# Kernel tuning notes

Hardware: AMD Instinct MI355X
Metric: run time of the kernel (lower is better)

## Reference

```python
import jax, jax.numpy as jnp
import numpy as np
from jax import lax

DIM = 512
HEADS = 8
HID = 128           # FRN hidden_dim
DIM_CONV = DIM // 4 # 128, partial-conv channels
EPS = 1e-5


def layernorm(x, g, b):
    mu = jnp.mean(x, axis=-1, keepdims=True)
    var = jnp.mean((x - mu) ** 2, axis=-1, keepdims=True)
    return (x - mu) * lax.rsqrt(var + EPS) * g + b


def conv2d(x, w, groups=1):
    # x: (N,C,H,W), w: (O, C/groups, kh, kw), stride 1, SAME padding
    return lax.conv_general_dilated(x, w, (1, 1), 'SAME',
                                    dimension_numbers=('NCHW', 'OIHW', 'NCHW'),
                                    feature_group_count=groups)


def setup_inputs() -> dict:
    key = jax.random.key(0)
    ks = jax.random.split(key, 12)
    s = 0.02
    inp = {
        'x': jax.random.normal(ks[0], (196, 256, DIM), dtype=jnp.float32),
        'ln1_g': jnp.ones((DIM,), jnp.float32),
        'ln1_b': jnp.zeros((DIM,), jnp.float32),
        'qkv_w': jax.random.normal(ks[1], (DIM, 3 * DIM), jnp.float32) * s,
        'proj_w': jax.random.normal(ks[2], (DIM, DIM), jnp.float32) * s,
        'proj_b': jnp.zeros((DIM,), jnp.float32),
        'ln2_g': jnp.ones((DIM,), jnp.float32),
        'ln2_b': jnp.zeros((DIM,), jnp.float32),
        'pconv_w': jax.random.normal(ks[3], (DIM_CONV, DIM_CONV, 3, 3), jnp.float32) * s,
        'lin1_w': jax.random.normal(ks[4], (DIM, 2 * HID), jnp.float32) * s,
        'lin1_b': jnp.zeros((2 * HID,), jnp.float32),
        'dw_w': jax.random.normal(ks[5], (HID, 1, 3, 3), jnp.float32) * s,
        'dw_b': jnp.zeros((HID,), jnp.float32),
        'lin2_w': jax.random.normal(ks[6], (HID, DIM), jnp.float32) * s,
        'lin2_b': jnp.zeros((DIM,), jnp.float32),
    }
    return inp


def reference(x, ln1_g, ln1_b, qkv_w, proj_w, proj_b, ln2_g, ln2_b,
              pconv_w, lin1_w, lin1_b, dw_w, dw_b, lin2_w, lin2_b):
    B, N, C = x.shape
    hd = C // HEADS
    scale = hd ** -0.5

    # ---- SQAttention on norm1(x) ----
    h = layernorm(x, ln1_g, ln1_b)
    qkv = (h @ qkv_w).reshape(B, N, 3, HEADS, hd)
    q, k, v = qkv[:, :, 0], qkv[:, :, 1], qkv[:, :, 2]  # (B,N,H,hd)
    attn = jnp.einsum('bnhd,bmhd->bhnm', q, k) * scale   # (B,H,N,N)
    # sigmoid mask from the LAST query row, averaged over heads
    mask = jax.nn.sigmoid(jnp.mean(attn[:, :, -1, :], axis=1))[:, None, None, :]  # (B,1,1,N)
    attn = jax.nn.softmax(attn, axis=-1) * mask
    o = jnp.einsum('bhnm,bmhd->bnhd', attn, v).reshape(B, N, C)
    x = x + (o @ proj_w + proj_b)

    # ---- FRN on norm2(x): treats axis0 as (h w)=hw, axis1 as batch ----
    y = layernorm(x, ln2_g, ln2_b)
    hw, bs, c = y.shape
    hh = int(np.sqrt(hw))
    yi = y.reshape(hh, hh, bs, c).transpose(2, 3, 0, 1)  # (bs,c,hh,hh)
    y1 = conv2d(yi[:, :DIM_CONV], pconv_w)               # partial conv, no bias
    yi = jnp.concatenate([y1, yi[:, DIM_CONV:]], axis=1)
    y = yi.transpose(2, 3, 0, 1).reshape(hw, bs, c)      # (hw,bs,c)
    y = jax.nn.gelu(y @ lin1_w + lin1_b, approximate=False)
    y_1, y_2 = y[..., :HID], y[..., HID:]
    y1i = y_1.reshape(hh, hh, bs, HID).transpose(2, 3, 0, 1)
    y1i = jax.nn.gelu(conv2d(y1i, dw_w, groups=HID) + dw_b[None, :, None, None],
                      approximate=False)
    y_1 = y1i.transpose(2, 3, 0, 1).reshape(hw, bs, HID)
    y = (y_1 * y_2) @ lin2_w + lin2_b
    return x + y
```

## Files before the change

### kernel.cpp

```cpp
#include <hip/hip_runtime.h>
#include <hip/hip_bf16.h>

#define NB   196
#define NT   256
#define CDIM 512
#define NH   8
#define MROWS 50176
#define HB   98
#define MH   (HB*NT)

typedef __attribute__((ext_vector_type(8))) short short8;
typedef __attribute__((ext_vector_type(4))) float f32x4;
typedef __attribute__((ext_vector_type(4))) unsigned uint32x4;

__device__ __forceinline__ float gelu_f(float x) {
    return 0.5f * x * (1.0f + erff(x * 0.70710678118654752440f));
}
__device__ __forceinline__ float b2f(unsigned u) { return __uint_as_float(u << 16); }
__device__ __forceinline__ unsigned f2b(float f) {
    __hip_bfloat16 h = __float2bfloat16(f);
    return (unsigned)__builtin_bit_cast(unsigned short, h);
}
__device__ __forceinline__ unsigned pk2(float a, float b) { return f2b(a) | (f2b(b) << 16); }
__device__ __forceinline__ void u4_to_f8(uint4 v, float* f) {
    f[0] = b2f(v.x & 0xffffu); f[1] = b2f(v.x >> 16);
    f[2] = b2f(v.y & 0xffffu); f[3] = b2f(v.y >> 16);
    f[4] = b2f(v.z & 0xffffu); f[5] = b2f(v.z >> 16);
    f[6] = b2f(v.w & 0xffffu); f[7] = b2f(v.w >> 16);
}
__device__ __forceinline__ void gload_lds16(const void* g, void* l) {
    __builtin_amdgcn_global_load_lds(
        (const __attribute__((address_space(1))) void*)g,
        (__attribute__((address_space(3))) void*)l, 16, 0, 0);
}
static inline int xcd_grid(int NBM, int NBN) { return 8 * ((NBM + 7) / 8) * NBN; }

__global__ __launch_bounds__(256) void convert_wT_kernel(
    const float* __restrict__ w, unsigned short* __restrict__ wT, int K, int N)
{
    int o = blockIdx.x * 256 + threadIdx.x;
    if (o >= K * N) return;
    int k = o / N, n = o - k * N;
    wT[(size_t)n * K + k] = (unsigned short)f2b(w[o]);
}
__global__ __launch_bounds__(256) void convert_kernel(
    const float* __restrict__ w, unsigned short* __restrict__ wT, int n)
{
    int o = blockIdx.x * 256 + threadIdx.x;
    if (o < n) wT[o] = (unsigned short)f2b(w[o]);
}

template<int INBF>
__global__ __launch_bounds__(64) void ln_kernel(
    const void* __restrict__ inp, const float* __restrict__ g,
    const float* __restrict__ b, unsigned short* __restrict__ out)
{
    int row = blockIdx.x;
    int lane = threadIdx.x;
    float f[8];
    if constexpr (INBF) {
        const unsigned short* p = (const unsigned short*)inp + (size_t)row * CDIM + lane * 8;
        uint4 v = *(const uint4*)p;
        u4_to_f8(v, f);
    } else {
        const float* p = (const float*)inp + (size_t)row * CDIM + lane * 8;
        float4 a = *(const float4*)p;
        float4 c = *(const float4*)(p + 4);
        f[0]=a.x; f[1]=a.y; f[2]=a.z; f[3]=a.w; f[4]=c.x; f[5]=c.y; f[6]=c.z; f[7]=c.w;
    }
    float s = 0;
#pragma unroll
    for (int i = 0; i < 8; ++i) s += f[i];
#pragma unroll
    for (int off = 1; off < 64; off <<= 1) s += __shfl_xor(s, off);
    float mu = s * (1.0f / 512.0f);
    float sq = 0;
#pragma unroll
    for (int i = 0; i < 8; ++i) { f[i] -= mu; sq += f[i] * f[i]; }
#pragma unroll
    for (int off = 1; off < 64; off <<= 1) sq += __shfl_xor(sq, off);
    float inv = rsqrtf(sq * (1.0f / 512.0f) + 1e-5f);
    float4 g0 = *(const float4*)(g + lane * 8);
    float4 g1 = *(const float4*)(g + lane * 8 + 4);
    float4 b0 = *(const float4*)(b + lane * 8);
    float4 b1 = *(const float4*)(b + lane * 8 + 4);
    float r0 = f[0]*inv*g0.x + b0.x, r1 = f[1]*inv*g0.y + b0.y;
    float r2 = f[2]*inv*g0.z + b0.z, r3 = f[3]*inv*g0.w + b0.w;
    float r4 = f[4]*inv*g1.x + b1.x, r5 = f[5]*inv*g1.y + b1.y;
    float r6 = f[6]*inv*g1.z + b1.z, r7 = f[7]*inv*g1.w + b1.w;
    uint4 ov = { pk2(r0, r1), pk2(r2, r3), pk2(r4, r5), pk2(r6, r7) };
    *(uint4*)(out + (size_t)row * CDIM + lane * 8) = ov;
}

#define QUAD16(MH, NH) \
    __builtin_amdgcn_s_setprio(1); \
    _Pragma("unroll") \
    for (int mi2 = 0; mi2 < 4; ++mi2) \
        _Pragma("unroll") \
        for (int nj2 = 0; nj2 < 2; ++nj2) \
            _Pragma("unroll") \
            for (int kk = 0; kk < 2; ++kk) \
                acc[(MH)*4 + mi2][(NH)*2 + nj2] = __builtin_amdgcn_mfma_f32_16x16x32_bf16( \
                    afr[mi2][kk], bfr[nj2][kk], acc[(MH)*4 + mi2][(NH)*2 + nj2], 0, 0, 0); \
    __builtin_amdgcn_s_setprio(0);

template<typename TC, int RES>
__global__ __launch_bounds__(512, 2) void gemm_mfma256(
    const unsigned short* __restrict__ A,
    const unsigned short* __restrict__ BT,
    const float* __restrict__ bias,
    const void* __restrict__ resid,
    TC* __restrict__ C,
    int K, int lda, int ldc, int act, int NBM, int NBN)
{
    __shared__ __align__(16) unsigned short As[2][256][64];
    __shared__ __align__(16) unsigned short Bs[2][256][64];
    int lin = blockIdx.x;
    int xcd = lin & 7;
    int rr = lin >> 3;
    int nb = rr % NBN;
    int pb = rr / NBN;
    int mb = (pb << 3) + xcd;
    if (mb >= NBM) return;
    int m0 = mb << 8;
    int n0 = nb << 8;

    int tid = threadIdx.x;
    int lane = tid & 63;
    int wave = tid >> 6;
    int wr = wave >> 2;
    int wc = wave & 3;
    int fr = lane & 15;
    int fg = lane >> 4;

    int rsub8 = lane >> 3;
    int cch = lane & 7;

    auto stage = [&](int p, int k0) {
#pragma unroll
        for (int tI = 0; tI < 4; ++tI) {
            int seg = (wave << 2) + tI;
            int row = (seg << 3) + rsub8;
            int csrc = (cch ^ (row & 7)) << 3;
            gload_lds16(A + (size_t)(m0 + row) * lda + k0 + csrc,
                        (char*)&As[p][0][0] + (seg << 10));
        }
#pragma unroll
        for (int tI = 0; tI < 4; ++tI) {
            int seg = (wave << 2) + tI;
            int row = (seg << 3) + rsub8;
            int csrc = (cch ^ (row & 7)) << 3;
            gload_lds16(BT + (size_t)(n0 + row) * K + k0 + csrc,
                        (char*)&Bs[p][0][0] + (seg << 10));
        }
    };

    f32x4 acc[8][4];
#pragma unroll
    for (int i = 0; i < 8; ++i)
#pragma unroll
        for (int j = 0; j < 4; ++j) acc[i][j] = (f32x4){0.f, 0.f, 0.f, 0.f};

    short8 afr[4][2];
    short8 bfr[2][2];

    auto loadA = [&](int p, int mh) {
#pragma unroll
        for (int mi2 = 0; mi2 < 4; ++mi2)
#pragma unroll
            for (int kk = 0; kk < 2; ++kk) {
                int row = (wr << 7) + (mh << 6) + (mi2 << 4) + fr;
                int ch = ((kk << 2) + fg) ^ (row & 7);
                afr[mi2][kk] = *(const short8*)&As[p][row][ch << 3];
            }
    };
    auto loadB = [&](int p, int nh) {
#pragma unroll
        for (int nj2 = 0; nj2 < 2; ++nj2)
#pragma unroll
            for (int kk = 0; kk < 2; ++kk) {
                int row = (wc << 6) + (nh << 5) + (nj2 << 4) + fr;
                int ch = ((kk << 2) + fg) ^ (row & 7);
                bfr[nj2][kk] = *(const short8*)&Bs[p][row][ch << 3];
            }
    };

    int NKT = K >> 6;
    stage(0, 0);
    asm volatile("s_waitcnt vmcnt(0)" ::: "memory");
    __builtin_amdgcn_s_barrier();

    for (int t = 0; t < NKT; ++t) {
        int p = t & 1;
        if (t + 1 < NKT) stage(p ^ 1, (t + 1) << 6);
        loadA(p, 0); loadB(p, 0);
        QUAD16(0, 0)
        __builtin_amdgcn_s_barrier();
        loadB(p, 1);
        QUAD16(0, 1)
        __builtin_amdgcn_s_barrier();
        loadA(p, 1);
        QUAD16(1, 1)
        __builtin_amdgcn_s_barrier();
        loadB(p, 0);
        QUAD16(1, 0)
        if (t + 1 < NKT) asm volatile("s_waitcnt vmcnt(0)" ::: "memory");
        __builtin_amdgcn_s_barrier();
    }

#pragma unroll
    for (int mi = 0; mi < 8; ++mi) {
        int rowb = m0 + (wr << 7) + (mi << 4) + (fg << 2);
#pragma unroll
        for (int nj = 0; nj < 4; ++nj) {
            int col = n0 + (wc << 6) + (nj << 4) + fr;
            float bj = bias ? bias[col] : 0.0f;
#pragma unroll
            for (int r = 0; r < 4; ++r) {
                int row = rowb + r;
                float v = acc[mi][nj][r] + bj;
                if constexpr (RES == 1)
                    v += ((const float*)resid)[(size_t)row * ldc + col];
                else if constexpr (RES == 2)
                    v += b2f(((const unsigned short*)resid)[(size_t)row * ldc + col]);
                if (act) v = gelu_f(v);
                if constexpr (sizeof(TC) == 4)
                    ((float*)C)[(size_t)row * ldc + col] = v;
                else
                    ((unsigned short*)C)[(size_t)row * ldc + col] = (unsigned short)f2b(v);
            }
        }
    }
}

template<typename TC, int RES, int CONV>
__global__ __launch_bounds__(256) void gemm_mfma(
    const unsigned short* __restrict__ A,
    const unsigned short* __restrict__ BT,
    const float* __restrict__ bias,
    const void* __restrict__ resid,
    TC* __restrict__ C,
    int K, int lda, int ldc, int act, int NBM, int NBN)
{
    __shared__ __align__(16) unsigned short As[3][128][32];
    __shared__ __align__(16) unsigned short Bs[3][128][32];
    int lin = blockIdx.x;
    int xcd = lin & 7;
    int rr = lin >> 3;
    int nb = rr % NBN;
    int pb = rr / NBN;
    int mb = (pb << 3) + xcd;
    if (mb >= NBM) return;
    int m0 = mb << 7;
    int n0 = nb << 7;

    int tid = threadIdx.x;
    int lane = tid & 63;
    int wave = tid >> 6;
    int wr = wave >> 1, wc = wave & 1;
    int fr = lane & 15;
    int fg = lane >> 4;

    int rsub = lane >> 2;
    int cch = lane & 3;
    int csrc = (cch ^ (rsub & 3)) << 3;

    int i0 = 0, j0 = 0, bs0 = 0;
    if constexpr (CONV) {
        int hw = m0 >> 8;
        i0 = hw / 14; j0 = hw - i0 * 14;
        bs0 = m0 & 255;
    }

    auto stage = [&](int bf, int k0) {
        if constexpr (CONV) {
            int kl = tid & 31;
            int mq = (tid >> 5) << 4;
            int k = k0 + kl;
            int ci = k / 9; int r9 = k - ci * 9;
            int di = r9 / 3; int dj = r9 - di * 3;
            int ii = i0 + di - 1, jj = j0 + dj - 1;
            uint4 v0 = {0,0,0,0}, v1 = {0,0,0,0};
            if ((unsigned)ii < 14u && (unsigned)jj < 14u) {
                const unsigned short* src = A + (size_t)ci * MROWS + (size_t)(ii * 14 + jj) * 256 + bs0 + mq;
                v0 = *(const uint4*)src;
                v1 = *(const uint4*)(src + 8);
            }
            unsigned short e[16];
            *(uint4*)&e[0] = v0; *(uint4*)&e[8] = v1;
            int ch = kl >> 3, wi = kl & 7;
#pragma unroll
            for (int e2 = 0; e2 < 16; ++e2)
                As[bf][mq + e2][((ch ^ (e2 & 3)) << 3) + wi] = e[e2];
        } else {
#pragma unroll
            for (int t = 0; t < 2; ++t) {
                int seg = (wave << 1) + t;
                int row = (seg << 4) + rsub;
                gload_lds16(A + (size_t)(m0 + row) * lda + k0 + csrc,
                            (char*)&As[bf][0][0] + (seg << 10));
            }
        }
#pragma unroll
        for (int t = 0; t < 2; ++t) {
            int seg = (wave << 1) + t;
            int row = (seg << 4) + rsub;
            gload_lds16(BT + (size_t)(n0 + row) * K + k0 + csrc,
                        (char*)&Bs[bf][0][0] + (seg << 10));
        }
    };

    f32x4 acc[4][4];
#pragma unroll
    for (int i = 0; i < 4; ++i)
#pragma unroll
        for (int j = 0; j < 4; ++j) acc[i][j] = (f32x4){0.f, 0.f, 0.f, 0.f};

    int nsteps = K >> 5;
    stage(0, 0);
    if (nsteps > 1) {
        stage(1, 32);
        asm volatile("s_waitcnt vmcnt(4)" ::: "memory");
    } else {
        asm volatile("s_waitcnt vmcnt(0)" ::: "memory");
    }
    __builtin_amdgcn_s_barrier();

    for (int s = 0; s < nsteps; ++s) {
        int bcur = s % 3;
        if (s + 2 < nsteps) stage((s + 2) % 3, (s + 2) << 5);
        int chl = (fg ^ (fr & 3)) << 3;
        short8 af[4], bfr[4];
#pragma unroll
        for (int i = 0; i < 4; ++i)
            af[i] = *(const short8*)&As[bcur][(wr << 6) + (i << 4) + fr][chl];
#pragma unroll
        for (int j = 0; j < 4; ++j)
            bfr[j] = *(const short8*)&Bs[bcur][(wc << 6) + (j << 4) + fr][chl];
#pragma unroll
        for (int i = 0; i < 4; ++i)
#pragma unroll
            for (int j = 0; j < 4; ++j)
                acc[i][j] = __builtin_amdgcn_mfma_f32_16x16x32_bf16(af[i], bfr[j], acc[i][j], 0, 0, 0);
        if (s + 1 < nsteps) {
            if (s + 2 < nsteps) asm volatile("s_waitcnt vmcnt(4) lgkmcnt(0)" ::: "memory");
            else                asm volatile("s_waitcnt vmcnt(0) lgkmcnt(0)" ::: "memory");
            __builtin_amdgcn_s_barrier();
        }
    }

#pragma unroll
    for (int i = 0; i < 4; ++i) {
        int rowb = m0 + (wr << 6) + (i << 4) + ((lane >> 4) << 2);
#pragma unroll
        for (int j = 0; j < 4; ++j) {
            int col = n0 + (wc << 6) + (j << 4) + fr;
            float bj = bias ? bias[col] : 0.0f;
#pragma unroll
            for (int r = 0; r < 4; ++r) {
                int row = rowb + r;
                float v = acc[i][j][r] + bj;
                if constexpr (RES == 1)
                    v += ((const float*)resid)[(size_t)row * ldc + col];
                else if constexpr (RES == 2)
                    v += b2f(((const unsigned short*)resid)[(size_t)row * ldc + col]);
                if (act) v = gelu_f(v);
                if constexpr (sizeof(TC) == 4)
                    ((float*)C)[(size_t)row * ldc + col] = v;
                else
                    ((unsigned short*)C)[(size_t)row * ldc + col] = (unsigned short)f2b(v);
            }
        }
    }
}

__global__ __launch_bounds__(256) void mask_kernel(
    const unsigned short* __restrict__ qkv, float* __restrict__ mk)
{
    __shared__ float ql[512];
    int b = blockIdx.x, tid = threadIdx.x;
    const unsigned short* qlast = qkv + ((size_t)(b * NT + 255) * 3) * CDIM;
    ql[tid] = b2f(qlast[tid]);
    ql[tid + 256] = b2f(qlast[tid + 256]);
    __syncthreads();
    const unsigned short* kp = qkv + ((size_t)(b * NT + tid) * 3 + 1) * CDIM;
    float s = 0;
    for (int cq = 0; cq < 512; cq += 8) {
        uint4 kv = *(const uint4*)(kp + cq);
        float f[8];
        u4_to_f8(kv, f);
#pragma unroll
        for (int q = 0; q < 8; ++q) s += ql[cq + q] * f[q];
    }
    s *= 0.015625f;
    mk[b * NT + tid] = 1.0f / (1.0f + __expf(-s));
}

__global__ __launch_bounds__(512) void attn_mfma(
    const unsigned short* __restrict__ qkv, const float* __restrict__ mask,
    unsigned short* __restrict__ o)
{
    __shared__ __align__(16) unsigned short smem[128][64];
    int h = blockIdx.x, b = blockIdx.y;
    int tid = threadIdx.x;
    int lane = tid & 63;
    int wid = tid >> 6;
    int fr = lane & 15;
    int fg = lane >> 4;
    const unsigned short* base = qkv + (size_t)b * NT * 3 * CDIM + h * 64;

    short8 qf[2][2];
#pragma unroll
    for (int t = 0; t < 2; ++t)
#pragma unroll
        for (int kc = 0; kc < 2; ++kc)
            qf[t][kc] = *(const short8*)(base +
                (size_t)((wid << 5) + (t << 4) + fr) * 3 * CDIM + (kc << 5) + (fg << 3));

    f32x4 oacc[2][4];
#pragma unroll
    for (int t = 0; t < 2; ++t)
#pragma unroll
        for (int n = 0; n < 4; ++n) oacc[t][n] = (f32x4){0.f, 0.f, 0.f, 0.f};
    float l[2] = {0.f, 0.f};

    int srcA = ((fg & 1) << 5) + fr;

    for (int c = 0; c < 4; ++c) {
        __syncthreads();
        {
            int kr = tid >> 3, ch = tid & 7;
            int gm = (c << 6) + kr;
            uint4 kv = *(const uint4*)(base + (size_t)(gm * 3 + 1) * CDIM + (ch << 3));
            *(uint4*)&smem[kr][(ch ^ (kr & 7)) << 3] = kv;
            float mv = mask[b * NT + gm];
            uint4 vv = *(const uint4*)(base + (size_t)(gm * 3 + 2) * CDIM + (ch << 3));
            float f[8];
            u4_to_f8(vv, f);
#pragma unroll
            for (int e = 0; e < 8; ++e) {
                int d = (ch << 3) + e;
                smem[64 + d][(((kr >> 3) ^ (d & 7)) << 3) + (kr & 7)] = (unsigned short)f2b(f[e] * mv);
            }
        }
        __syncthreads();
        short8 kf[4][2];
#pragma unroll
        for (int j = 0; j < 4; ++j)
#pragma unroll
            for (int kc = 0; kc < 2; ++kc)
                kf[j][kc] = *(const short8*)&smem[(j << 4) + fr][((((kc << 2) + fg) ^ (fr & 7)) << 3)];
        short8 vf[4][2];
#pragma unroll
        for (int n = 0; n < 4; ++n)
#pragma unroll
            for (int kc2 = 0; kc2 < 2; ++kc2)
                vf[n][kc2] = *(const short8*)&smem[64 + (n << 4) + fr][((((kc2 << 2) + fg) ^ (fr & 7)) << 3)];
#pragma unroll
        for (int t = 0; t < 2; ++t) {
            f32x4 sa[4];
#pragma unroll
            for (int j = 0; j < 4; ++j) sa[j] = (f32x4){0.f, 0.f, 0.f, 0.f};
#pragma unroll
            for (int kc = 0; kc < 2; ++kc)
#pragma unroll
                for (int j = 0; j < 4; ++j)
                    sa[j] = __builtin_amdgcn_mfma_f32_16x16x32_bf16(kf[j][kc], qf[t][kc], sa[j], 0, 0, 0);
            float p[4][4];
            float ls = 0.f;
#pragma unroll
            for (int j = 0; j < 4; ++j)
#pragma unroll
                for (int r = 0; r < 4; ++r) {
                    p[j][r] = __expf(sa[j][r] * 0.125f);
                    ls += p[j][r];
                }
            ls += __shfl_xor(ls, 16);
            ls += __shfl_xor(ls, 32);
            l[t] += ls;
            unsigned pkv[4][2];
#pragma unroll
            for (int j = 0; j < 4; ++j) {
                pkv[j][0] = pk2(p[j][0], p[j][1]);
                pkv[j][1] = pk2(p[j][2], p[j][3]);
            }
#pragma unroll
            for (int kc2 = 0; kc2 < 2; ++kc2) {
                unsigned w0[4], w1[4];
                w0[0] = __shfl(pkv[(kc2 << 1) + 0][0], srcA);
                w0[1] = __shfl(pkv[(kc2 << 1) + 0][1], srcA);
                w0[2] = __shfl(pkv[(kc2 << 1) + 0][0], srcA + 16);
                w0[3] = __shfl(pkv[(kc2 << 1) + 0][1], srcA + 16);
                w1[0] = __shfl(pkv[(kc2 << 1) + 1][0], srcA);
                w1[1] = __shfl(pkv[(kc2 << 1) + 1][1], srcA);
                w1[2] = __shfl(pkv[(kc2 << 1) + 1][0], srcA + 16);
                w1[3] = __shfl(pkv[(kc2 << 1) + 1][1], srcA + 16);
                bool hi = fg >= 2;
                uint32x4 pw = { hi ? w1[0] : w0[0], hi ? w1[1] : w0[1],
                                hi ? w1[2] : w0[2], hi ? w1[3] : w0[3] };
                short8 pf = __builtin_bit_cast(short8, pw);
#pragma unroll
                for (int n = 0; n < 4; ++n)
                    oacc[t][n] = __builtin_amdgcn_mfma_f32_16x16x32_bf16(pf, vf[n][kc2], oacc[t][n], 0, 0, 0);
            }
        }
    }

#pragma unroll
    for (int half = 0; half < 2; ++half) {
        __syncthreads();
        if ((wid >> 2) == half) {
            int qr = (wid & 3) << 5;
#pragma unroll
            for (int t = 0; t < 2; ++t) {
                float invl = 1.0f / l[t];
                float rl[4];
#pragma unroll
                for (int r = 0; r < 4; ++r)
                    rl[r] = __shfl(invl, (fg << 2) + r);
#pragma unroll
                for (int n = 0; n < 4; ++n)
#pragma unroll
                    for (int r = 0; r < 4; ++r) {
                        int row = qr + (t << 4) + (fg << 2) + r;
                        int d = (n << 4) + fr;
                        smem[row][((((d >> 3) ^ (row & 7)) << 3)) | (d & 7)] =
                            (unsigned short)f2b(oacc[t][n][r] * rl[r]);
                    }
            }
        }
        __syncthreads();
#pragma unroll
        for (int p = 0; p < 2; ++p) {
            int idx = tid + (p << 9);
            int row = idx >> 3;
            int ch = idx & 7;
            uint4 ov = *(const uint4*)&smem[row][(ch ^ (row & 7)) << 3];
            *(uint4*)(o + (size_t)(b * NT + (half << 7) + row) * CDIM + h * 64 + (ch << 3)) = ov;
        }
    }
}

__global__ __launch_bounds__(256) void transpose_kernel(
    const unsigned short* __restrict__ y, unsigned short* __restrict__ yT)
{
    int g = blockIdx.x * 256 + threadIdx.x;
    int row = g >> 4;
    int cq = (g & 15) << 3;
    uint4 v = *(const uint4*)(y + (size_t)row * CDIM + cq);
    unsigned short e[8] = {
        (unsigned short)(v.x & 0xffffu), (unsigned short)(v.x >> 16),
        (unsigned short)(v.y & 0xffffu), (unsigned short)(v.y >> 16),
        (unsigned short)(v.z & 0xffffu), (unsigned short)(v.z >> 16),
        (unsigned short)(v.w & 0xffffu), (unsigned short)(v.w >> 16) };
    int hw = row >> 8, bs = row & 255;
    size_t off = (size_t)cq * MROWS + (size_t)hw * 256 + bs;
#pragma unroll
    for (int i = 0; i < 8; ++i) yT[off + (size_t)i * MROWS] = e[i];
}

__global__ __launch_bounds__(256) void dwconv_kernel(
    const unsigned short* __restrict__ u, const float* __restrict__ w,
    const float* __restrict__ wb, unsigned short* __restrict__ y1)
{
    int hw = blockIdx.x;
    int i = hw / 14;
    int j = hw - i * 14;
    int tid = threadIdx.x;
    int c = (tid & 31) << 2;
    int bs = (blockIdx.y << 3) + (tid >> 5);
    float a0 = 0, a1 = 0, a2 = 0, a3 = 0;
#pragma unroll
    for (int di = 0; di < 3; ++di) {
        int ii = i + di - 1;
        if ((unsigned)ii >= 14u) continue;
#pragma unroll
        for (int dj = 0; dj < 3; ++dj) {
            int jj = j + dj - 1;
            if ((unsigned)jj >= 14u) continue;
            int r = di * 3 + dj;
            uint2 uv = *(const uint2*)(u + ((size_t)(ii * 14 + jj) * 256 + bs) * 256 + c);
            a0 += w[(c + 0) * 9 + r] * b2f(uv.x & 0xffffu);
            a1 += w[(c + 1) * 9 + r] * b2f(uv.x >> 16);
            a2 += w[(c + 2) * 9 + r] * b2f(uv.y & 0xffffu);
            a3 += w[(c + 3) * 9 + r] * b2f(uv.y >> 16);
        }
    }
    a0 = gelu_f(a0 + wb[c]);
    a1 = gelu_f(a1 + wb[c + 1]);
    a2 = gelu_f(a2 + wb[c + 2]);
    a3 = gelu_f(a3 + wb[c + 3]);
    uint2 g2 = *(const uint2*)(u + ((size_t)hw * 256 + bs) * 256 + 128 + c);
    a0 *= b2f(g2.x & 0xffffu); a1 *= b2f(g2.x >> 16);
    a2 *= b2f(g2.y & 0xffffu); a3 *= b2f(g2.y >> 16);
    ushort4 ov = { (unsigned short)f2b(a0), (unsigned short)f2b(a1),
                   (unsigned short)f2b(a2), (unsigned short)f2b(a3) };
    *(ushort4*)(y1 + ((size_t)hw * 256 + bs) * 128 + c) = ov;
}

extern "C" void kernel_launch(void* const* d_in, const int* in_sizes, int n_in,
                              void* d_out, int out_size, void* d_ws, size_t ws_size,
                              hipStream_t stream)
{
    (void)in_sizes; (void)n_in; (void)out_size; (void)ws_size;
    const float* x      = (const float*)d_in[0];
    const float* ln1_g  = (const float*)d_in[1];
    const float* ln1_b  = (const float*)d_in[2];
    const float* qkv_w  = (const float*)d_in[3];
    const float* proj_w = (const float*)d_in[4];
    const float* proj_b = (const float*)d_in[5];
    const float* ln2_g  = (const float*)d_in[6];
    const float* ln2_b  = (const float*)d_in[7];
    const float* pconv_w= (const float*)d_in[8];
    const float* lin1_w = (const float*)d_in[9];
    const float* lin1_b = (const float*)d_in[10];
    const float* dw_w   = (const float*)d_in[11];
    const float* dw_b   = (const float*)d_in[12];
    const float* lin2_w = (const float*)d_in[13];
    const float* lin2_b = (const float*)d_in[14];
    float* out = (float*)d_out;

    unsigned short* Ob   = (unsigned short*)d_out;
    unsigned short* o_bf = Ob;
    unsigned short* h_bf = Ob + 25690112;
    float* mk            = (float*)(Ob + 25690112 + 12845056);
    unsigned short* y_bf = Ob;
    unsigned short* yT_b = Ob + 25690112;

    unsigned short* ws16   = (unsigned short*)d_ws;
    unsigned short* qkvW   = ws16;
    unsigned short* projW  = ws16 + 786432;
    unsigned short* pconvW = ws16 + 1048576;
    unsigned short* lin1W  = ws16 + 1196032;
    unsigned short* lin2W  = ws16 + 1327104;
    unsigned short* qkv_b  = ws16 + 1392640;
    unsigned short* x2_b   = ws16 + 1392640;
    unsigned short* u_b    = ws16 + 27082752;
    unsigned short* y1_b   = ws16 + 39927808;

    convert_wT_kernel<<<3072, 256, 0, stream>>>(qkv_w,  qkvW,  512, 1536);
    convert_wT_kernel<<<1024, 256, 0, stream>>>(proj_w, projW, 512, 512);
    convert_kernel  <<< 576, 256, 0, stream>>>(pconv_w, pconvW, 147456);
    convert_wT_kernel<<< 512, 256, 0, stream>>>(lin1_w, lin1W, 512, 256);
    convert_wT_kernel<<< 256, 256, 0, stream>>>(lin2_w, lin2W, 128, 512);

    for (int r = 0; r < 2; ++r) {
        const float* xr = x + (size_t)r * MH * CDIM;
        ln_kernel<0><<<MH, 64, 0, stream>>>(xr, ln1_g, ln1_b, h_bf);
        gemm_mfma256<unsigned short, 0><<<xcd_grid(98, 6), 512, 0, stream>>>(
            h_bf, qkvW, nullptr, nullptr, qkv_b, 512, 512, 1536, 0, 98, 6);
        mask_kernel<<<HB, 256, 0, stream>>>(qkv_b, mk + (size_t)r * HB * NT);
        attn_mfma<<<dim3(NH, HB), 512, 0, stream>>>(
            qkv_b, mk + (size_t)r * HB * NT, o_bf + (size_t)r * MH * CDIM);
    }
    gemm_mfma256<unsigned short, 1><<<xcd_grid(196, 2), 512, 0, stream>>>(
        o_bf, projW, proj_b, x, x2_b, 512, 512, 512, 0, 196, 2);
    ln_kernel<1><<<MROWS, 64, 0, stream>>>(x2_b, ln2_g, ln2_b, y_bf);
    transpose_kernel<<<3136, 256, 0, stream>>>(y_bf, yT_b);
    gemm_mfma<unsigned short, 0, 1><<<xcd_grid(392, 1), 256, 0, stream>>>(
        yT_b, pconvW, nullptr, nullptr, y_bf, 1152, 0, 512, 0, 392, 1);
    gemm_mfma256<unsigned short, 0><<<xcd_grid(196, 1), 512, 0, stream>>>(
        y_bf, lin1W, lin1_b, nullptr, u_b, 512, 512, 256, 1, 196, 1);
    dwconv_kernel<<<dim3(NB, 32), 256, 0, stream>>>(u_b, dw_w, dw_b, y1_b);
    gemm_mfma256<float, 2><<<xcd_grid(196, 2), 512, 0, stream>>>(
        y1_b, lin2W, lin2_b, x2_b, out, 128, 128, 512, 0, 196, 2);
}
```

Baseline: 855.1 us.

## Split next-tile global-to-LDS staging into four chunks interleaved with MFMA phases

Prefetching of the next K tile is broken into four chunks: the two A halves and the two B halves. Each chunk is issued in a different compute phase, and the phase barriers become partial `vmcnt(4)` waits, so a phase only waits for the data it actually consumes. This replaces a full `vmcnt(0)` drain at the end of every iteration, with the aim of spreading memory traffic evenly and overlapping it with MFMA work. Launch bounds also drop from 2 to 1 blocks per CU, which gives the compiler more registers; the 128 KB of LDS per block already limited occupancy to one block.

Measured after the change: 895.7 us. 1.05x slower.

```diff
diff --git a/kernel.cpp b/kernel.cpp
--- a/kernel.cpp
+++ b/kernel.cpp
@@ -104,8 +104,13 @@
                     afr[mi2][kk], bfr[nj2][kk], acc[(MH)*4 + mi2][(NH)*2 + nj2], 0, 0, 0); \
     __builtin_amdgcn_s_setprio(0);
 
+#define PHASE_WAIT() \
+    if (pre) asm volatile("s_waitcnt vmcnt(4)" ::: "memory"); \
+    else     asm volatile("s_waitcnt vmcnt(0)" ::: "memory"); \
+    __builtin_amdgcn_s_barrier();
+
 template<typename TC, int RES>
-__global__ __launch_bounds__(512, 2) void gemm_mfma256(
+__global__ __launch_bounds__(512, 1) void gemm_mfma256(
     const unsigned short* __restrict__ A,
     const unsigned short* __restrict__ BT,
     const float* __restrict__ bias,
@@ -133,25 +138,25 @@
     int fr = lane & 15;
     int fg = lane >> 4;
 
-    int rsub8 = lane >> 3;
-    int cch = lane & 7;
-
-    auto stage = [&](int p, int k0) {
-#pragma unroll
-        for (int tI = 0; tI < 4; ++tI) {
-            int seg = (wave << 2) + tI;
-            int row = (seg << 3) + rsub8;
-            int csrc = (cch ^ (row & 7)) << 3;
-            gload_lds16(A + (size_t)(m0 + row) * lda + k0 + csrc,
-                        (char*)&As[p][0][0] + (seg << 10));
-        }
-#pragma unroll
-        for (int tI = 0; tI < 4; ++tI) {
-            int seg = (wave << 2) + tI;
-            int row = (seg << 3) + rsub8;
-            int csrc = (cch ^ (row & 7)) << 3;
-            gload_lds16(BT + (size_t)(n0 + row) * K + k0 + csrc,
-                        (char*)&Bs[p][0][0] + (seg << 10));
+    auto stage_chunk = [&](int p, int k0, int type) {
+        const unsigned short* SRC;
+        char* LBASE;
+        int seg, ld, base0;
+        if (type == 0 || type == 3) {
+            SRC = A; LBASE = (char*)&As[p][0][0]; ld = lda; base0 = m0;
+            seg = (type == 0) ? ((wave < 4) ? wave : wave + 4)
+                              : ((wave < 4) ? wave + 4 : wave + 8);
+        } else {
+            SRC = BT; LBASE = (char*)&Bs[p][0][0]; ld = K; base0 = n0;
+            seg = ((wave >> 1) << 2) + (wave & 1) + ((type == 2) ? 2 : 0);
+        }
+#pragma unroll
+        for (int i = 0; i < 2; ++i) {
+            int row = (seg << 4) + (i << 3) + (lane >> 3);
+            int c = lane & 7;
+            int csrc = ((c ^ (row & 7)) << 3);
+            gload_lds16(SRC + (size_t)(base0 + row) * ld + k0 + csrc,
+                        LBASE + (seg << 11) + (i << 10));
         }
     };
 
@@ -186,26 +191,31 @@
     };
 
     int NKT = K >> 6;
-    stage(0, 0);
-    asm volatile("s_waitcnt vmcnt(0)" ::: "memory");
+    stage_chunk(0, 0, 0); stage_chunk(0, 0, 1);
+    stage_chunk(0, 0, 2); stage_chunk(0, 0, 3);
+    asm volatile("s_waitcnt vmcnt(4)" ::: "memory");
     __builtin_amdgcn_s_barrier();
 
     for (int t = 0; t < NKT; ++t) {
         int p = t & 1;
-        if (t + 1 < NKT) stage(p ^ 1, (t + 1) << 6);
+        bool pre = (t + 1 < NKT);
+        int k1 = (t + 1) << 6;
+        if (pre) stage_chunk(p ^ 1, k1, 0);
         loadA(p, 0); loadB(p, 0);
         QUAD16(0, 0)
-        __builtin_amdgcn_s_barrier();
+        PHASE_WAIT()
+        if (pre) stage_chunk(p ^ 1, k1, 1);
         loadB(p, 1);
         QUAD16(0, 1)
-        __builtin_amdgcn_s_barrier();
+        PHASE_WAIT()
+        if (pre) stage_chunk(p ^ 1, k1, 2);
         loadA(p, 1);
         QUAD16(1, 1)
-        __builtin_amdgcn_s_barrier();
+        PHASE_WAIT()
+        if (pre) stage_chunk(p ^ 1, k1, 3);
         loadB(p, 0);
         QUAD16(1, 0)
-        if (t + 1 < NKT) asm volatile("s_waitcnt vmcnt(0)" ::: "memory");
-        __builtin_amdgcn_s_barrier();
+        PHASE_WAIT()
     }
 
 #pragma unroll
```
